# Kernel optimization log

Hardware: AMD Instinct MI355X
Metric: run time of the kernel (lower is better)

## Reference

```python
import jax, jax.numpy as jnp
import numpy as np

N = 100000
EPS_BN = 1e-5


def setup_inputs() -> dict:
    key = jax.random.key(0)
    ks = jax.random.split(key, 12)
    x = jax.random.normal(ks[0], (N, 128), dtype=jnp.float32)
    edge_index = jax.random.randint(ks[1], (2, 800000), 0, N, dtype=jnp.int64)
    # GCNConv layer params (PyG: lin weight [out,in], bias added after aggregation)
    s = 1.0 / np.sqrt(128.0)
    W1 = jax.random.uniform(ks[2], (128, 128), jnp.float32, -s, s)
    b1 = jnp.zeros((128,), jnp.float32)
    W2 = jax.random.uniform(ks[3], (128, 128), jnp.float32, -s, s)
    b2 = jnp.zeros((128,), jnp.float32)
    # BatchNorm affine params
    g1 = jnp.ones((128,), jnp.float32)
    be1 = jnp.zeros((128,), jnp.float32)
    g2 = jnp.ones((128,), jnp.float32)
    be2 = jnp.zeros((128,), jnp.float32)
    # PReLU single shared parameter (torch init = 0.25)
    a = jnp.asarray(0.25, jnp.float32)
    return {"x": x, "edge_index": edge_index, "W1": W1, "b1": b1, "g1": g1,
            "be1": be1, "W2": W2, "b2": b2, "g2": g2, "be2": be2, "a": a}


def _gcn_conv(x, src, dst, deg_inv_sqrt, W, b):
    # x' = D^-1/2 (A+I) D^-1/2 (x W^T) + b  (self loops already in src/dst)
    h = x @ W.T                                   # [N, out]
    norm = deg_inv_sqrt[src] * deg_inv_sqrt[dst]  # [E+N]
    msg = h[src] * norm[:, None]                  # gather + scale
    out = jax.ops.segment_sum(msg, dst, num_segments=N)  # scatter-add
    return out + b


def _batchnorm(x, g, be):
    # training-mode BatchNorm1d over nodes (biased variance)
    mean = jnp.mean(x, axis=0)
    var = jnp.mean(jnp.square(x - mean), axis=0)
    return (x - mean) * jax.lax.rsqrt(var + EPS_BN) * g + be


def _prelu(x, a):
    return jnp.where(x > 0, x, a * x)


def reference(x, edge_index, W1, b1, g1, be1, W2, b2, g2, be2, a):
    # add self loops
    loops = jnp.arange(N, dtype=edge_index.dtype)
    src = jnp.concatenate([edge_index[0], loops])
    dst = jnp.concatenate([edge_index[1], loops])
    # symmetric normalization from in-degree at destinations
    deg = jax.ops.segment_sum(jnp.ones_like(dst, dtype=x.dtype), dst, num_segments=N)
    deg_inv_sqrt = jnp.where(deg > 0, jax.lax.rsqrt(deg), 0.0)

    h = _gcn_conv(x, src, dst, deg_inv_sqrt, W1, b1)
    h = _prelu(_batchnorm(h, g1, be1), a)
    h = _gcn_conv(h, src, dst, deg_inv_sqrt, W2, b2)
    h = _prelu(_batchnorm(h, g2, be2), a)
    return h
```

## Files before the change

### kernel.cpp

```cpp
#include <hip/hip_runtime.h>
#include <cstddef>
#include <cstdint>


#define EPS_BN 1e-5f

typedef short short8 __attribute__((ext_vector_type(8)));
typedef float f32x4 __attribute__((ext_vector_type(4)));

static __device__ __forceinline__ unsigned short f2b(float f) {
    union { float f; uint32_t u; } v; v.f = f;
    uint32_t u = v.u;
    return (unsigned short)((u + 0x7FFFu + ((u >> 16) & 1u)) >> 16);
}
static __device__ __forceinline__ float b2f(unsigned short h) {
    union { uint32_t u; float f; } v; v.u = ((uint32_t)h) << 16;
    return v.f;
}
static __device__ __forceinline__ float b2f_s(short h) { return b2f((unsigned short)h); }

__global__ __launch_bounds__(256) void k_prep(const float* __restrict__ W1, const float* __restrict__ W2,
                                              unsigned short* __restrict__ Wz1, unsigned short* __restrict__ Wz2,
                                              const int* __restrict__ dst, int* __restrict__ cnt,
                                              int* __restrict__ rank, int E) {
    int bid = blockIdx.x, tid = threadIdx.x;
    if (bid < 128) {
        int gi = bid * 256 + tid;
        const float* W = (gi < 16384) ? W1 : W2;
        unsigned short* Wz = (gi < 16384) ? Wz1 : Wz2;
        int idx = gi & 16383;
        int o = idx >> 7, k = idx & 127;
        int ct = o >> 4, nn = o & 15, ks = k >> 5, q = (k >> 3) & 3, j = k & 7;
        Wz[(ct * 4 + ks) * 512 + (q * 16 + nn) * 8 + j] = f2b(W[idx]);
    } else {
        int e = (bid - 128) * 256 + tid;
        if (e < E) rank[e] = atomicAdd(&cnt[dst[e]], 1);
    }
}

__global__ __launch_bounds__(256) void k_scanA(const int* __restrict__ cnt, int* __restrict__ partial, int n) {
    __shared__ int sd[256];
    int tid = threadIdx.x;
    int base = blockIdx.x * 1024 + tid * 4;
    int s = 0;
#pragma unroll
    for (int j = 0; j < 4; j++) { int idx = base + j; if (idx < n) s += cnt[idx]; }
    sd[tid] = s; __syncthreads();
    for (int off = 128; off > 0; off >>= 1) {
        if (tid < off) sd[tid] += sd[tid + off];
        __syncthreads();
    }
    if (tid == 0) partial[blockIdx.x] = sd[0];
}

__global__ __launch_bounds__(256) void k_scanC(const int* __restrict__ cnt, const int* __restrict__ partial,
                                               int* __restrict__ rowptr, float* __restrict__ dis, int n, int nb) {
    __shared__ int sp[256];
    __shared__ int sd[256];
    int tid = threadIdx.x;
    sp[tid] = (tid < nb) ? partial[tid] : 0;
    int base = blockIdx.x * 1024 + tid * 4;
    int v[4]; int s = 0;
#pragma unroll
    for (int j = 0; j < 4; j++) { int idx = base + j; v[j] = (idx < n) ? cnt[idx] : 0; s += v[j]; }
    sd[tid] = s;
    __syncthreads();
    for (int off = 1; off < 256; off <<= 1) {
        int a = (tid >= off) ? sp[tid - off] : 0;
        int b = (tid >= off) ? sd[tid - off] : 0;
        __syncthreads();
        sp[tid] += a; sd[tid] += b;
        __syncthreads();
    }
    int gbase = (blockIdx.x == 0) ? 0 : sp[blockIdx.x - 1];
    int excl = gbase + ((tid == 0) ? 0 : sd[tid - 1]);
#pragma unroll
    for (int j = 0; j < 4; j++) {
        int idx = base + j;
        if (idx < n) {
            rowptr[idx] = excl;
            dis[idx] = rsqrtf((float)(v[j] + 1));
        }
        excl += v[j];
    }
}

__global__ __launch_bounds__(256) void k_fill_gemm1(const float* __restrict__ X,
                                                    const unsigned short* __restrict__ Wz,
                                                    unsigned short* __restrict__ Yb, int n,
                                                    const int* __restrict__ src, const int* __restrict__ dst,
                                                    const int* __restrict__ rowptr, const int* __restrict__ rank,
                                                    int* __restrict__ colw, int E, int gGemm) {
    __shared__ unsigned short lds[16384];
    int tid = threadIdx.x;
    if ((int)blockIdx.x >= gGemm) {
        int e = (blockIdx.x - gGemm) * 256 + tid;
        if (e < E) {
            int d = dst[e];
            colw[rowptr[d] + rank[e]] = src[e];
        }
        return;
    }
    const short8* wsrc = (const short8*)Wz;
    short8* ldst = (short8*)lds;
#pragma unroll
    for (int i = 0; i < 8; i++) ldst[tid + 256 * i] = wsrc[tid + 256 * i];
    __syncthreads();

    int wave = tid >> 6, lane = tid & 63;
    int r0 = blockIdx.x * 64 + wave * 16;
    int mrow = lane & 15, quad = lane >> 4;
    int arow = r0 + mrow; if (arow > n - 1) arow = n - 1;
    const float* xr = X + (size_t)arow * 128;

    f32x4 acc[8];
#pragma unroll
    for (int ct = 0; ct < 8; ct++) acc[ct] = (f32x4){0.f, 0.f, 0.f, 0.f};

#pragma unroll
    for (int ks = 0; ks < 4; ks++) {
        int kb = ks * 32 + quad * 8;
        float4 x0 = *reinterpret_cast<const float4*>(xr + kb);
        float4 x1 = *reinterpret_cast<const float4*>(xr + kb + 4);
        short8 a;
        a[0] = (short)f2b(x0.x); a[1] = (short)f2b(x0.y); a[2] = (short)f2b(x0.z); a[3] = (short)f2b(x0.w);
        a[4] = (short)f2b(x1.x); a[5] = (short)f2b(x1.y); a[6] = (short)f2b(x1.z); a[7] = (short)f2b(x1.w);
#pragma unroll
        for (int ct = 0; ct < 8; ct++) {
            short8 b = *(const short8*)(lds + (ct * 4 + ks) * 512 + lane * 8);
            acc[ct] = __builtin_amdgcn_mfma_f32_16x16x32_bf16(a, b, acc[ct], 0, 0, 0);
        }
    }
#pragma unroll
    for (int i = 0; i < 4; i++) {
        int row = r0 + quad * 4 + i;
        if (row < n) {
#pragma unroll
            for (int ct = 0; ct < 8; ct++)
                Yb[(size_t)row * 128 + ct * 16 + mrow] = f2b(acc[ct][i]);
        }
    }
}

__global__ __launch_bounds__(256) void k_gemm2(const unsigned short* __restrict__ Ab,
                                               const unsigned short* __restrict__ Wz,
                                               const float* __restrict__ acc1,
                                               const float* __restrict__ g1, const float* __restrict__ be1,
                                               const float* __restrict__ ap,
                                               unsigned short* __restrict__ Yb, float invN, int n) {
    __shared__ unsigned short lds[16384];
    __shared__ float scl[128];
    __shared__ float shl[128];
    int tid = threadIdx.x;
    if (tid < 128) {
        float mean = acc1[tid] * invN;
        float var = acc1[128 + tid] * invN - mean * mean;
        float rstd = rsqrtf(var + EPS_BN);
        float scale = g1[tid] * rstd;
        scl[tid] = scale;
        shl[tid] = fmaf(-mean, scale, be1[tid]);
    }
    const short8* wsrc = (const short8*)Wz;
    short8* ldst = (short8*)lds;
#pragma unroll
    for (int i = 0; i < 8; i++) ldst[tid + 256 * i] = wsrc[tid + 256 * i];
    __syncthreads();

    float alpha = ap[0];
    int wave = tid >> 6, lane = tid & 63;
    int r0 = blockIdx.x * 64 + wave * 16;
    int mrow = lane & 15, quad = lane >> 4;
    int arow = r0 + mrow; if (arow > n - 1) arow = n - 1;
    const unsigned short* ar = Ab + (size_t)arow * 128;

    f32x4 acc[8];
#pragma unroll
    for (int ct = 0; ct < 8; ct++) acc[ct] = (f32x4){0.f, 0.f, 0.f, 0.f};

#pragma unroll
    for (int ks = 0; ks < 4; ks++) {
        int kb = ks * 32 + quad * 8;
        short8 raw = *(const short8*)(ar + kb);
        float4 s0 = *reinterpret_cast<const float4*>(scl + kb);
        float4 s1 = *reinterpret_cast<const float4*>(scl + kb + 4);
        float4 t0 = *reinterpret_cast<const float4*>(shl + kb);
        float4 t1 = *reinterpret_cast<const float4*>(shl + kb + 4);
        float ss[8] = {s0.x, s0.y, s0.z, s0.w, s1.x, s1.y, s1.z, s1.w};
        float tt[8] = {t0.x, t0.y, t0.z, t0.w, t1.x, t1.y, t1.z, t1.w};
        short8 a;
#pragma unroll
        for (int j = 0; j < 8; j++) {
            float x = fmaf(b2f_s(raw[j]), ss[j], tt[j]);
            x = x > 0.f ? x : alpha * x;
            a[j] = (short)f2b(x);
        }
#pragma unroll
        for (int ct = 0; ct < 8; ct++) {
            short8 b = *(const short8*)(lds + (ct * 4 + ks) * 512 + lane * 8);
            acc[ct] = __builtin_amdgcn_mfma_f32_16x16x32_bf16(a, b, acc[ct], 0, 0, 0);
        }
    }
#pragma unroll
    for (int i = 0; i < 4; i++) {
        int row = r0 + quad * 4 + i;
        if (row < n) {
#pragma unroll
            for (int ct = 0; ct < 8; ct++)
                Yb[(size_t)row * 128 + ct * 16 + mrow] = f2b(acc[ct][i]);
        }
    }
}

__global__ __launch_bounds__(256) void k_aggst(const unsigned short* __restrict__ Hb,
                                               const int* __restrict__ rowptr, const int* __restrict__ cnt,
                                               const int* __restrict__ colw, const float* __restrict__ dis,
                                               const float* __restrict__ bias,
                                               unsigned short* __restrict__ outb,
                                               float* __restrict__ part, int n) {
    __shared__ float ls[4][128];
    __shared__ float lq[4][128];
    int tid = threadIdx.x;
    int lane = tid & 15, slot = tid >> 4;
    int node = blockIdx.x * 16 + slot;
    bool act = node < n;
    int nodec = act ? node : (n - 1);
    int lo = lane * 8;
    float dn = dis[nodec];
    short8 hv = *(const short8*)(Hb + (size_t)nodec * 128 + lo);
    float acc[8];
#pragma unroll
    for (int j = 0; j < 8; j++) acc[j] = dn * b2f_s(hv[j]);
    int num = act ? cnt[nodec] : 0;
    int beg = rowptr[nodec];
    const int* cw = colw + beg;
    int e = 0;
    for (; e + 4 <= num; e += 4) {
        int s0 = cw[e], s1 = cw[e + 1], s2 = cw[e + 2], s3 = cw[e + 3];
        float w0 = dis[s0], w1 = dis[s1], w2 = dis[s2], w3 = dis[s3];
        short8 n0 = *(const short8*)(Hb + (size_t)s0 * 128 + lo);
        short8 n1 = *(const short8*)(Hb + (size_t)s1 * 128 + lo);
        short8 n2 = *(const short8*)(Hb + (size_t)s2 * 128 + lo);
        short8 n3 = *(const short8*)(Hb + (size_t)s3 * 128 + lo);
#pragma unroll
        for (int j = 0; j < 8; j++) {
            acc[j] = fmaf(w0, b2f_s(n0[j]), acc[j]);
            acc[j] = fmaf(w1, b2f_s(n1[j]), acc[j]);
            acc[j] = fmaf(w2, b2f_s(n2[j]), acc[j]);
            acc[j] = fmaf(w3, b2f_s(n3[j]), acc[j]);
        }
    }
    for (; e < num; ++e) {
        int s = cw[e];
        float w = dis[s];
        short8 nb = *(const short8*)(Hb + (size_t)s * 128 + lo);
#pragma unroll
        for (int j = 0; j < 8; j++) acc[j] = fmaf(w, b2f_s(nb[j]), acc[j]);
    }
    const float4 bv0 = reinterpret_cast<const float4*>(bias)[lane * 2 + 0];
    const float4 bv1 = reinterpret_cast<const float4*>(bias)[lane * 2 + 1];
    float bb[8] = {bv0.x, bv0.y, bv0.z, bv0.w, bv1.x, bv1.y, bv1.z, bv1.w};
    short8 ov;
    float s8[8], q8[8];
#pragma unroll
    for (int j = 0; j < 8; j++) {
        float y = fmaf(dn, acc[j], bb[j]);
        unsigned short h = f2b(y);
        ov[j] = (short)h;
        float fv = act ? b2f(h) : 0.f;
        s8[j] = fv;
        q8[j] = fv * fv;
    }
    if (act) *(short8*)(outb + (size_t)node * 128 + lo) = ov;
#pragma unroll
    for (int j = 0; j < 8; j++) {
        s8[j] += __shfl_xor(s8[j], 16, 64);
        q8[j] += __shfl_xor(q8[j], 16, 64);
        s8[j] += __shfl_xor(s8[j], 32, 64);
        q8[j] += __shfl_xor(q8[j], 32, 64);
    }
    int wave = tid >> 6;
    if ((tid & 63) < 16) {
#pragma unroll
        for (int j = 0; j < 8; j++) {
            ls[wave][lane * 8 + j] = s8[j];
            lq[wave][lane * 8 + j] = q8[j];
        }
    }
    __syncthreads();
    if (tid < 128) {
        float r = ls[0][tid] + ls[1][tid] + ls[2][tid] + ls[3][tid];
        part[(size_t)blockIdx.x * 256 + tid] = r;
    } else {
        int f = tid - 128;
        float r = lq[0][f] + lq[1][f] + lq[2][f] + lq[3][f];
        part[(size_t)blockIdx.x * 256 + 128 + f] = r;
    }
}

__global__ __launch_bounds__(256) void k_bnred(const float* __restrict__ part, float* __restrict__ acc, int nb) {
    int tid = threadIdx.x;
    float s = 0.f;
    for (int b = blockIdx.x; b < nb; b += gridDim.x) s += part[(size_t)b * 256 + tid];
    atomicAdd(&acc[tid], s);
}

__global__ __launch_bounds__(256) void k_bnact_f(const unsigned short* __restrict__ X, float* __restrict__ Y,
                                                 const float* __restrict__ acc2,
                                                 const float* __restrict__ g2, const float* __restrict__ be2,
                                                 const float* __restrict__ ap, float invN, int n8) {
    __shared__ float scl[128];
    __shared__ float shl[128];
    int tid = threadIdx.x;
    if (tid < 128) {
        float mean = acc2[tid] * invN;
        float var = acc2[128 + tid] * invN - mean * mean;
        float rstd = rsqrtf(var + EPS_BN);
        float scale = g2[tid] * rstd;
        scl[tid] = scale;
        shl[tid] = fmaf(-mean, scale, be2[tid]);
    }
    __syncthreads();
    int i = blockIdx.x * 256 + tid;
    if (i >= n8) return;
    float a = ap[0];
    int g = i & 15;
    const float4 s0 = reinterpret_cast<const float4*>(scl)[g * 2 + 0];
    const float4 s1 = reinterpret_cast<const float4*>(scl)[g * 2 + 1];
    const float4 t0 = reinterpret_cast<const float4*>(shl)[g * 2 + 0];
    const float4 t1 = reinterpret_cast<const float4*>(shl)[g * 2 + 1];
    float ss[8] = {s0.x, s0.y, s0.z, s0.w, s1.x, s1.y, s1.z, s1.w};
    float tt[8] = {t0.x, t0.y, t0.z, t0.w, t1.x, t1.y, t1.z, t1.w};
    short8 v = reinterpret_cast<const short8*>(X)[i];
    float out[8];
#pragma unroll
    for (int j = 0; j < 8; j++) {
        float x = fmaf(b2f_s(v[j]), ss[j], tt[j]);
        out[j] = x > 0.f ? x : a * x;
    }
    float4 o0 = {out[0], out[1], out[2], out[3]};
    float4 o1 = {out[4], out[5], out[6], out[7]};
    reinterpret_cast<float4*>(Y)[i * 2 + 0] = o0;
    reinterpret_cast<float4*>(Y)[i * 2 + 1] = o1;
}

extern "C" void kernel_launch(void* const* d_in, const int* in_sizes, int n_in,
                              void* d_out, int out_size, void* d_ws, size_t ws_size,
                              hipStream_t stream) {
    (void)n_in; (void)out_size; (void)ws_size;
    const float* x   = (const float*)d_in[0];
    const int*   ei  = (const int*)d_in[1];
    const float* W1  = (const float*)d_in[2];
    const float* b1  = (const float*)d_in[3];
    const float* g1  = (const float*)d_in[4];
    const float* be1 = (const float*)d_in[5];
    const float* W2  = (const float*)d_in[6];
    const float* b2  = (const float*)d_in[7];
    const float* g2  = (const float*)d_in[8];
    const float* be2 = (const float*)d_in[9];
    const float* ap  = (const float*)d_in[10];
    float* out = (float*)d_out;

    const int N = in_sizes[0] / 128;
    const int E = in_sizes[1] / 2;
    const int* srcIdx = ei;
    const int* dstIdx = ei + E;

    const int NB = (N + 1023) / 1024;
    const int gE = (E + 255) / 256;
    const int n8 = N * 16;
    const int gGemm = (N + 63) / 64;
    const int gAgg  = (N + 15) / 16;

    char* w = (char*)d_ws;
    size_t off = 0;
    auto alloc = [&](size_t bytes) { char* p = w + off; off += (bytes + 255) & ~(size_t)255; return p; };
    int*   cnt     = (int*)  alloc((size_t)N * 4);
    float* acc1    = (float*)alloc(1024);
    float* acc2    = (float*)alloc(1024);
    size_t zero_bytes = off;
    int*   rowptr  = (int*)  alloc((size_t)N * 4);
    int*   rank    = (int*)  alloc((size_t)E * 4);
    int*   colw    = (int*)  alloc((size_t)E * 4);
    float* dis     = (float*)alloc((size_t)N * 4);
    int*   partial = (int*)  alloc(4096);
    float* part    = (float*)alloc((size_t)gAgg * 256 * 4);
    unsigned short* Wz1 = (unsigned short*)alloc(16384 * 2);
    unsigned short* Wz2 = (unsigned short*)alloc(16384 * 2);
    unsigned short* bufH = (unsigned short*)alloc((size_t)N * 128 * 2);
    unsigned short* bufA = (unsigned short*)alloc((size_t)N * 128 * 2);

    const float invN = 1.0f / (float)N;

    hipMemsetAsync(cnt, 0, zero_bytes, stream);

    k_prep<<<128 + gE, 256, 0, stream>>>(W1, W2, Wz1, Wz2, dstIdx, cnt, rank, E);

    k_scanA<<<NB, 256, 0, stream>>>(cnt, partial, N);
    k_scanC<<<NB, 256, 0, stream>>>(cnt, partial, rowptr, dis, N, NB);

    k_fill_gemm1<<<gGemm + gE, 256, 0, stream>>>(x, Wz1, bufH, N,
                                                 srcIdx, dstIdx, rowptr, rank, colw, E, gGemm);
    k_aggst<<<gAgg, 256, 0, stream>>>(bufH, rowptr, cnt, colw, dis, b1, bufA, part, N);
    k_bnred<<<64, 256, 0, stream>>>(part, acc1, gAgg);

    k_gemm2<<<gGemm, 256, 0, stream>>>(bufA, Wz2, acc1, g1, be1, ap, bufH, invN, N);
    k_aggst<<<gAgg, 256, 0, stream>>>(bufH, rowptr, cnt, colw, dis, b2, bufA, part, N);
    k_bnred<<<64, 256, 0, stream>>>(part, acc2, gAgg);
    k_bnact_f<<<(n8 + 255) / 256, 256, 0, stream>>>(bufA, out, acc2, g2, be2, ap, invN, n8);
}
```

Before: 342.2 us.

## Fuse all stages into one persistent cooperative kernel with grid syncs

Replaces the chain of separate kernel launches (prep, scans, fill+GEMM1, aggregation, BN reduction, GEMM2, final BN/act) with a single cooperative persistent kernel that uses grid-wide barriers between phases and grid-stride loops. BN statistics are now accumulated per block across many nodes and atomically added directly, removing the partials buffer and the separate reduction kernels. This is meant to remove launch gaps and the extra partials traffic, but it adds grid.sync costs, limits the grid to occupancy-bound block counts, and uses a large static LDS allocation that may reduce occupancy. The scan phases now run on only a few blocks while all others wait at the barrier.

```diff
diff --git a/kernel.cpp b/kernel.cpp
--- a/kernel.cpp
+++ b/kernel.cpp
@@ -1,9 +1,12 @@
 #include <hip/hip_runtime.h>
+#include <hip/hip_cooperative_groups.h>
 #include <cstddef>
 #include <cstdint>
 
 
 #define EPS_BN 1e-5f
+
+namespace cg = cooperative_groups;
 
 typedef short short8 __attribute__((ext_vector_type(8)));
 typedef float f32x4 __attribute__((ext_vector_type(4)));
@@ -19,328 +22,336 @@
 }
 static __device__ __forceinline__ float b2f_s(short h) { return b2f((unsigned short)h); }
 
-__global__ __launch_bounds__(256) void k_prep(const float* __restrict__ W1, const float* __restrict__ W2,
-                                              unsigned short* __restrict__ Wz1, unsigned short* __restrict__ Wz2,
-                                              const int* __restrict__ dst, int* __restrict__ cnt,
-                                              int* __restrict__ rank, int E) {
-    int bid = blockIdx.x, tid = threadIdx.x;
-    if (bid < 128) {
-        int gi = bid * 256 + tid;
-        const float* W = (gi < 16384) ? W1 : W2;
-        unsigned short* Wz = (gi < 16384) ? Wz1 : Wz2;
+struct Args {
+    const float* x;
+    const int* src;
+    const int* dst;
+    const float* W1; const float* b1; const float* g1; const float* be1;
+    const float* W2; const float* b2; const float* g2; const float* be2;
+    const float* ap;
+    float* out;
+    int* cnt; float* acc1; float* acc2;
+    int* rowptr; int* rank; int* colw; float* dis; int* partial;
+    unsigned short* Wz1; unsigned short* Wz2;
+    unsigned short* bufH; unsigned short* bufA;
+    int N, E, NB, nTiles, gAgg, n8;
+    float invN;
+};
+
+static __device__ __forceinline__ void agg_phase(const Args& a,
+                                                 const unsigned short* __restrict__ Hb,
+                                                 const float* __restrict__ bias,
+                                                 unsigned short* __restrict__ outb,
+                                                 float* __restrict__ accg,
+                                                 unsigned char* smem,
+                                                 int tid, int bid, int nBlocks) {
+    float rs[8], rq[8];
+#pragma unroll
+    for (int j = 0; j < 8; j++) { rs[j] = 0.f; rq[j] = 0.f; }
+    int lane = tid & 15, slot = tid >> 4;
+    int lo = lane * 8;
+    const float4 bv0 = reinterpret_cast<const float4*>(bias)[lane * 2 + 0];
+    const float4 bv1 = reinterpret_cast<const float4*>(bias)[lane * 2 + 1];
+    float bb[8] = {bv0.x, bv0.y, bv0.z, bv0.w, bv1.x, bv1.y, bv1.z, bv1.w};
+
+    for (int gb = bid; gb < a.gAgg; gb += nBlocks) {
+        int node = gb * 16 + slot;
+        bool act = node < a.N;
+        int nodec = act ? node : (a.N - 1);
+        float dn = a.dis[nodec];
+        short8 hv = *(const short8*)(Hb + (size_t)nodec * 128 + lo);
+        float acc[8];
+#pragma unroll
+        for (int j = 0; j < 8; j++) acc[j] = dn * b2f_s(hv[j]);
+        int num = act ? a.cnt[nodec] : 0;
+        int beg = a.rowptr[nodec];
+        const int* cw = a.colw + beg;
+        int e = 0;
+        for (; e + 4 <= num; e += 4) {
+            int s0 = cw[e], s1 = cw[e + 1], s2 = cw[e + 2], s3 = cw[e + 3];
+            float w0 = a.dis[s0], w1 = a.dis[s1], w2 = a.dis[s2], w3 = a.dis[s3];
+            short8 n0 = *(const short8*)(Hb + (size_t)s0 * 128 + lo);
+            short8 n1 = *(const short8*)(Hb + (size_t)s1 * 128 + lo);
+            short8 n2 = *(const short8*)(Hb + (size_t)s2 * 128 + lo);
+            short8 n3 = *(const short8*)(Hb + (size_t)s3 * 128 + lo);
+#pragma unroll
+            for (int j = 0; j < 8; j++) {
+                acc[j] = fmaf(w0, b2f_s(n0[j]), acc[j]);
+                acc[j] = fmaf(w1, b2f_s(n1[j]), acc[j]);
+                acc[j] = fmaf(w2, b2f_s(n2[j]), acc[j]);
+                acc[j] = fmaf(w3, b2f_s(n3[j]), acc[j]);
+            }
+        }
+        for (; e < num; ++e) {
+            int s = cw[e];
+            float w = a.dis[s];
+            short8 nb = *(const short8*)(Hb + (size_t)s * 128 + lo);
+#pragma unroll
+            for (int j = 0; j < 8; j++) acc[j] = fmaf(w, b2f_s(nb[j]), acc[j]);
+        }
+        short8 ov;
+#pragma unroll
+        for (int j = 0; j < 8; j++) {
+            float y = fmaf(dn, acc[j], bb[j]);
+            unsigned short h = f2b(y);
+            ov[j] = (short)h;
+            float fv = act ? b2f(h) : 0.f;
+            rs[j] += fv;
+            rq[j] = fmaf(fv, fv, rq[j]);
+        }
+        if (act) *(short8*)(outb + (size_t)node * 128 + lo) = ov;
+    }
+#pragma unroll
+    for (int j = 0; j < 8; j++) {
+        rs[j] += __shfl_xor(rs[j], 16, 64);
+        rq[j] += __shfl_xor(rq[j], 16, 64);
+        rs[j] += __shfl_xor(rs[j], 32, 64);
+        rq[j] += __shfl_xor(rq[j], 32, 64);
+    }
+    float* lsf = (float*)smem;
+    float* lqf = lsf + 512;
+    int wv = tid >> 6;
+    __syncthreads();
+    if ((tid & 63) < 16) {
+#pragma unroll
+        for (int j = 0; j < 8; j++) {
+            lsf[wv * 128 + lane * 8 + j] = rs[j];
+            lqf[wv * 128 + lane * 8 + j] = rq[j];
+        }
+    }
+    __syncthreads();
+    if (tid < 128) {
+        atomicAdd(&accg[tid], lsf[tid] + lsf[128 + tid] + lsf[256 + tid] + lsf[384 + tid]);
+    } else {
+        int f = tid - 128;
+        atomicAdd(&accg[tid], lqf[f] + lqf[128 + f] + lqf[256 + f] + lqf[384 + f]);
+    }
+}
+
+__global__ __launch_bounds__(256, 4) void k_mega(Args a) {
+    cg::grid_group grid = cg::this_grid();
+    __shared__ __align__(16) unsigned char smem[33792];
+    int tid = threadIdx.x;
+    int bid = blockIdx.x;
+    int nBlocks = gridDim.x;
+    int gtid = bid * 256 + tid;
+    int gth = nBlocks * 256;
+
+    for (int gi = gtid; gi < 32768; gi += gth) {
+        const float* W = (gi < 16384) ? a.W1 : a.W2;
+        unsigned short* Wz = (gi < 16384) ? a.Wz1 : a.Wz2;
         int idx = gi & 16383;
         int o = idx >> 7, k = idx & 127;
         int ct = o >> 4, nn = o & 15, ks = k >> 5, q = (k >> 3) & 3, j = k & 7;
         Wz[(ct * 4 + ks) * 512 + (q * 16 + nn) * 8 + j] = f2b(W[idx]);
-    } else {
-        int e = (bid - 128) * 256 + tid;
-        if (e < E) rank[e] = atomicAdd(&cnt[dst[e]], 1);
-    }
-}
-
-__global__ __launch_bounds__(256) void k_scanA(const int* __restrict__ cnt, int* __restrict__ partial, int n) {
-    __shared__ int sd[256];
-    int tid = threadIdx.x;
-    int base = blockIdx.x * 1024 + tid * 4;
-    int s = 0;
-#pragma unroll
-    for (int j = 0; j < 4; j++) { int idx = base + j; if (idx < n) s += cnt[idx]; }
-    sd[tid] = s; __syncthreads();
-    for (int off = 128; off > 0; off >>= 1) {
-        if (tid < off) sd[tid] += sd[tid + off];
+    }
+    for (int e = gtid; e < a.E; e += gth)
+        a.rank[e] = atomicAdd(&a.cnt[a.dst[e]], 1);
+    grid.sync();
+
+    {
+        int* sdI = (int*)smem;
+        for (int v = bid; v < a.NB; v += nBlocks) {
+            int base = v * 1024 + tid * 4;
+            int s = 0;
+#pragma unroll
+            for (int j = 0; j < 4; j++) { int idx = base + j; if (idx < a.N) s += a.cnt[idx]; }
+            sdI[tid] = s; __syncthreads();
+            for (int off = 128; off > 0; off >>= 1) {
+                if (tid < off) sdI[tid] += sdI[tid + off];
+                __syncthreads();
+            }
+            if (tid == 0) a.partial[v] = sdI[0];
+            __syncthreads();
+        }
+    }
+    grid.sync();
+
+    {
+        int* sp = (int*)smem;
+        int* sd = sp + 256;
+        for (int v = bid; v < a.NB; v += nBlocks) {
+            sp[tid] = (tid < a.NB) ? a.partial[tid] : 0;
+            int base = v * 1024 + tid * 4;
+            int vv[4]; int s = 0;
+#pragma unroll
+            for (int j = 0; j < 4; j++) { int idx = base + j; vv[j] = (idx < a.N) ? a.cnt[idx] : 0; s += vv[j]; }
+            sd[tid] = s;
+            __syncthreads();
+            for (int off = 1; off < 256; off <<= 1) {
+                int A = (tid >= off) ? sp[tid - off] : 0;
+                int B = (tid >= off) ? sd[tid - off] : 0;
+                __syncthreads();
+                sp[tid] += A; sd[tid] += B;
+                __syncthreads();
+            }
+            int gbase = (v == 0) ? 0 : sp[v - 1];
+            int excl = gbase + ((tid == 0) ? 0 : sd[tid - 1]);
+#pragma unroll
+            for (int j = 0; j < 4; j++) {
+                int idx = base + j;
+                if (idx < a.N) {
+                    a.rowptr[idx] = excl;
+                    a.dis[idx] = rsqrtf((float)(vv[j] + 1));
+                }
+                excl += vv[j];
+            }
+            __syncthreads();
+        }
+    }
+    grid.sync();
+
+    for (int e = gtid; e < a.E; e += gth) {
+        int d = a.dst[e];
+        a.colw[a.rowptr[d] + a.rank[e]] = a.src[e];
+    }
+    {
+        short8* lds8 = (short8*)smem;
+        const short8* wsrc = (const short8*)a.Wz1;
+#pragma unroll
+        for (int i = 0; i < 8; i++) lds8[tid + 256 * i] = wsrc[tid + 256 * i];
         __syncthreads();
-    }
-    if (tid == 0) partial[blockIdx.x] = sd[0];
-}
-
-__global__ __launch_bounds__(256) void k_scanC(const int* __restrict__ cnt, const int* __restrict__ partial,
-                                               int* __restrict__ rowptr, float* __restrict__ dis, int n, int nb) {
-    __shared__ int sp[256];
-    __shared__ int sd[256];
-    int tid = threadIdx.x;
-    sp[tid] = (tid < nb) ? partial[tid] : 0;
-    int base = blockIdx.x * 1024 + tid * 4;
-    int v[4]; int s = 0;
-#pragma unroll
-    for (int j = 0; j < 4; j++) { int idx = base + j; v[j] = (idx < n) ? cnt[idx] : 0; s += v[j]; }
-    sd[tid] = s;
-    __syncthreads();
-    for (int off = 1; off < 256; off <<= 1) {
-        int a = (tid >= off) ? sp[tid - off] : 0;
-        int b = (tid >= off) ? sd[tid - off] : 0;
+        unsigned short* ldsu = (unsigned short*)smem;
+        int wave = tid >> 6, lane = tid & 63;
+        int mrow = lane & 15, quad = lane >> 4;
+        for (int t = bid; t < a.nTiles; t += nBlocks) {
+            int r0 = t * 64 + wave * 16;
+            int arow = r0 + mrow; if (arow > a.N - 1) arow = a.N - 1;
+            const float* xr = a.x + (size_t)arow * 128;
+            f32x4 acc[8];
+#pragma unroll
+            for (int ct = 0; ct < 8; ct++) acc[ct] = (f32x4){0.f, 0.f, 0.f, 0.f};
+#pragma unroll
+            for (int ks = 0; ks < 4; ks++) {
+                int kb = ks * 32 + quad * 8;
+                float4 x0 = *reinterpret_cast<const float4*>(xr + kb);
+                float4 x1 = *reinterpret_cast<const float4*>(xr + kb + 4);
+                short8 av;
+                av[0] = (short)f2b(x0.x); av[1] = (short)f2b(x0.y); av[2] = (short)f2b(x0.z); av[3] = (short)f2b(x0.w);
+                av[4] = (short)f2b(x1.x); av[5] = (short)f2b(x1.y); av[6] = (short)f2b(x1.z); av[7] = (short)f2b(x1.w);
+#pragma unroll
+                for (int ct = 0; ct < 8; ct++) {
+                    short8 b = *(const short8*)(ldsu + (ct * 4 + ks) * 512 + lane * 8);
+                    acc[ct] = __builtin_amdgcn_mfma_f32_16x16x32_bf16(av, b, acc[ct], 0, 0, 0);
+                }
+            }
+#pragma unroll
+            for (int i = 0; i < 4; i++) {
+                int row = r0 + quad * 4 + i;
+                if (row < a.N) {
+#pragma unroll
+                    for (int ct = 0; ct < 8; ct++)
+                        a.bufH[(size_t)row * 128 + ct * 16 + mrow] = f2b(acc[ct][i]);
+                }
+            }
+        }
+    }
+    grid.sync();
+
+    agg_phase(a, a.bufH, a.b1, a.bufA, a.acc1, smem, tid, bid, nBlocks);
+    grid.sync();
+
+    {
+        float* scl = (float*)(smem + 32768);
+        float* shl = scl + 128;
+        if (tid < 128) {
+            float mean = a.acc1[tid] * a.invN;
+            float var = a.acc1[128 + tid] * a.invN - mean * mean;
+            float rstd = rsqrtf(var + EPS_BN);
+            float sc = a.g1[tid] * rstd;
+            scl[tid] = sc;
+            shl[tid] = fmaf(-mean, sc, a.be1[tid]);
+        }
+        short8* lds8 = (short8*)smem;
+        const short8* wsrc = (const short8*)a.Wz2;
+#pragma unroll
+        for (int i = 0; i < 8; i++) lds8[tid + 256 * i] = wsrc[tid + 256 * i];
         __syncthreads();
-        sp[tid] += a; sd[tid] += b;
+        unsigned short* ldsu = (unsigned short*)smem;
+        float alpha = a.ap[0];
+        int wave = tid >> 6, lane = tid & 63;
+        int mrow = lane & 15, quad = lane >> 4;
+        for (int t = bid; t < a.nTiles; t += nBlocks) {
+            int r0 = t * 64 + wave * 16;
+            int arow = r0 + mrow; if (arow > a.N - 1) arow = a.N - 1;
+            const unsigned short* ar = a.bufA + (size_t)arow * 128;
+            f32x4 acc[8];
+#pragma unroll
+            for (int ct = 0; ct < 8; ct++) acc[ct] = (f32x4){0.f, 0.f, 0.f, 0.f};
+#pragma unroll
+            for (int ks = 0; ks < 4; ks++) {
+                int kb = ks * 32 + quad * 8;
+                short8 raw = *(const short8*)(ar + kb);
+                float4 s0 = *reinterpret_cast<const float4*>(scl + kb);
+                float4 s1 = *reinterpret_cast<const float4*>(scl + kb + 4);
+                float4 t0 = *reinterpret_cast<const float4*>(shl + kb);
+                float4 t1 = *reinterpret_cast<const float4*>(shl + kb + 4);
+                float ss[8] = {s0.x, s0.y, s0.z, s0.w, s1.x, s1.y, s1.z, s1.w};
+                float tt[8] = {t0.x, t0.y, t0.z, t0.w, t1.x, t1.y, t1.z, t1.w};
+                short8 av;
+#pragma unroll
+                for (int j = 0; j < 8; j++) {
+                    float xv = fmaf(b2f_s(raw[j]), ss[j], tt[j]);
+                    xv = xv > 0.f ? xv : alpha * xv;
+                    av[j] = (short)f2b(xv);
+                }
+#pragma unroll
+                for (int ct = 0; ct < 8; ct++) {
+                    short8 b = *(const short8*)(ldsu + (ct * 4 + ks) * 512 + lane * 8);
+                    acc[ct] = __builtin_amdgcn_mfma_f32_16x16x32_bf16(av, b, acc[ct], 0, 0, 0);
+                }
+            }
+#pragma unroll
+            for (int i = 0; i < 4; i++) {
+                int row = r0 + quad * 4 + i;
+                if (row < a.N) {
+#pragma unroll
+                    for (int ct = 0; ct < 8; ct++)
+                        a.bufH[(size_t)row * 128 + ct * 16 + mrow] = f2b(acc[ct][i]);
+                }
+            }
+        }
+    }
+    grid.sync();
+
+    agg_phase(a, a.bufH, a.b2, a.bufA, a.acc2, smem, tid, bid, nBlocks);
+    grid.sync();
+
+    {
+        float* scl = (float*)smem;
+        float* shl = scl + 128;
         __syncthreads();
-    }
-    int gbase = (blockIdx.x == 0) ? 0 : sp[blockIdx.x - 1];
-    int excl = gbase + ((tid == 0) ? 0 : sd[tid - 1]);
-#pragma unroll
-    for (int j = 0; j < 4; j++) {
-        int idx = base + j;
-        if (idx < n) {
-            rowptr[idx] = excl;
-            dis[idx] = rsqrtf((float)(v[j] + 1));
-        }
-        excl += v[j];
-    }
-}
-
-__global__ __launch_bounds__(256) void k_fill_gemm1(const float* __restrict__ X,
-                                                    const unsigned short* __restrict__ Wz,
-                                                    unsigned short* __restrict__ Yb, int n,
-                                                    const int* __restrict__ src, const int* __restrict__ dst,
-                                                    const int* __restrict__ rowptr, const int* __restrict__ rank,
-                                                    int* __restrict__ colw, int E, int gGemm) {
-    __shared__ unsigned short lds[16384];
-    int tid = threadIdx.x;
-    if ((int)blockIdx.x >= gGemm) {
-        int e = (blockIdx.x - gGemm) * 256 + tid;
-        if (e < E) {
-            int d = dst[e];
-            colw[rowptr[d] + rank[e]] = src[e];
-        }
-        return;
-    }
-    const short8* wsrc = (const short8*)Wz;
-    short8* ldst = (short8*)lds;
-#pragma unroll
-    for (int i = 0; i < 8; i++) ldst[tid + 256 * i] = wsrc[tid + 256 * i];
-    __syncthreads();
-
-    int wave = tid >> 6, lane = tid & 63;
-    int r0 = blockIdx.x * 64 + wave * 16;
-    int mrow = lane & 15, quad = lane >> 4;
-    int arow = r0 + mrow; if (arow > n - 1) arow = n - 1;
-    const float* xr = X + (size_t)arow * 128;
-
-    f32x4 acc[8];
-#pragma unroll
-    for (int ct = 0; ct < 8; ct++) acc[ct] = (f32x4){0.f, 0.f, 0.f, 0.f};
-
-#pragma unroll
-    for (int ks = 0; ks < 4; ks++) {
-        int kb = ks * 32 + quad * 8;
-        float4 x0 = *reinterpret_cast<const float4*>(xr + kb);
-        float4 x1 = *reinterpret_cast<const float4*>(xr + kb + 4);
-        short8 a;
-        a[0] = (short)f2b(x0.x); a[1] = (short)f2b(x0.y); a[2] = (short)f2b(x0.z); a[3] = (short)f2b(x0.w);
-        a[4] = (short)f2b(x1.x); a[5] = (short)f2b(x1.y); a[6] = (short)f2b(x1.z); a[7] = (short)f2b(x1.w);
-#pragma unroll
-        for (int ct = 0; ct < 8; ct++) {
-            short8 b = *(const short8*)(lds + (ct * 4 + ks) * 512 + lane * 8);
-            acc[ct] = __builtin_amdgcn_mfma_f32_16x16x32_bf16(a, b, acc[ct], 0, 0, 0);
-        }
-    }
-#pragma unroll
-    for (int i = 0; i < 4; i++) {
-        int row = r0 + quad * 4 + i;
-        if (row < n) {
-#pragma unroll
-            for (int ct = 0; ct < 8; ct++)
-                Yb[(size_t)row * 128 + ct * 16 + mrow] = f2b(acc[ct][i]);
-        }
-    }
-}
-
-__global__ __launch_bounds__(256) void k_gemm2(const unsigned short* __restrict__ Ab,
-                                               const unsigned short* __restrict__ Wz,
-                                               const float* __restrict__ acc1,
-                                               const float* __restrict__ g1, const float* __restrict__ be1,
-                                               const float* __restrict__ ap,
-                                               unsigned short* __restrict__ Yb, float invN, int n) {
-    __shared__ unsigned short lds[16384];
-    __shared__ float scl[128];
-    __shared__ float shl[128];
-    int tid = threadIdx.x;
-    if (tid < 128) {
-        float mean = acc1[tid] * invN;
-        float var = acc1[128 + tid] * invN - mean * mean;
-        float rstd = rsqrtf(var + EPS_BN);
-        float scale = g1[tid] * rstd;
-        scl[tid] = scale;
-        shl[tid] = fmaf(-mean, scale, be1[tid]);
-    }
-    const short8* wsrc = (const short8*)Wz;
-    short8* ldst = (short8*)lds;
-#pragma unroll
-    for (int i = 0; i < 8; i++) ldst[tid + 256 * i] = wsrc[tid + 256 * i];
-    __syncthreads();
-
-    float alpha = ap[0];
-    int wave = tid >> 6, lane = tid & 63;
-    int r0 = blockIdx.x * 64 + wave * 16;
-    int mrow = lane & 15, quad = lane >> 4;
-    int arow = r0 + mrow; if (arow > n - 1) arow = n - 1;
-    const unsigned short* ar = Ab + (size_t)arow * 128;
-
-    f32x4 acc[8];
-#pragma unroll
-    for (int ct = 0; ct < 8; ct++) acc[ct] = (f32x4){0.f, 0.f, 0.f, 0.f};
-
-#pragma unroll
-    for (int ks = 0; ks < 4; ks++) {
-        int kb = ks * 32 + quad * 8;
-        short8 raw = *(const short8*)(ar + kb);
-        float4 s0 = *reinterpret_cast<const float4*>(scl + kb);
-        float4 s1 = *reinterpret_cast<const float4*>(scl + kb + 4);
-        float4 t0 = *reinterpret_cast<const float4*>(shl + kb);
-        float4 t1 = *reinterpret_cast<const float4*>(shl + kb + 4);
-        float ss[8] = {s0.x, s0.y, s0.z, s0.w, s1.x, s1.y, s1.z, s1.w};
-        float tt[8] = {t0.x, t0.y, t0.z, t0.w, t1.x, t1.y, t1.z, t1.w};
-        short8 a;
-#pragma unroll
-        for (int j = 0; j < 8; j++) {
-            float x = fmaf(b2f_s(raw[j]), ss[j], tt[j]);
-            x = x > 0.f ? x : alpha * x;
-            a[j] = (short)f2b(x);
-        }
-#pragma unroll
-        for (int ct = 0; ct < 8; ct++) {
-            short8 b = *(const short8*)(lds + (ct * 4 + ks) * 512 + lane * 8);
-            acc[ct] = __builtin_amdgcn_mfma_f32_16x16x32_bf16(a, b, acc[ct], 0, 0, 0);
-        }
-    }
-#pragma unroll
-    for (int i = 0; i < 4; i++) {
-        int row = r0 + quad * 4 + i;
-        if (row < n) {
-#pragma unroll
-            for (int ct = 0; ct < 8; ct++)
-                Yb[(size_t)row * 128 + ct * 16 + mrow] = f2b(acc[ct][i]);
-        }
-    }
-}
-
-__global__ __launch_bounds__(256) void k_aggst(const unsigned short* __restrict__ Hb,
-                                               const int* __restrict__ rowptr, const int* __restrict__ cnt,
-                                               const int* __restrict__ colw, const float* __restrict__ dis,
-                                               const float* __restrict__ bias,
-                                               unsigned short* __restrict__ outb,
-                                               float* __restrict__ part, int n) {
-    __shared__ float ls[4][128];
-    __shared__ float lq[4][128];
-    int tid = threadIdx.x;
-    int lane = tid & 15, slot = tid >> 4;
-    int node = blockIdx.x * 16 + slot;
-    bool act = node < n;
-    int nodec = act ? node : (n - 1);
-    int lo = lane * 8;
-    float dn = dis[nodec];
-    short8 hv = *(const short8*)(Hb + (size_t)nodec * 128 + lo);
-    float acc[8];
-#pragma unroll
-    for (int j = 0; j < 8; j++) acc[j] = dn * b2f_s(hv[j]);
-    int num = act ? cnt[nodec] : 0;
-    int beg = rowptr[nodec];
-    const int* cw = colw + beg;
-    int e = 0;
-    for (; e + 4 <= num; e += 4) {
-        int s0 = cw[e], s1 = cw[e + 1], s2 = cw[e + 2], s3 = cw[e + 3];
-        float w0 = dis[s0], w1 = dis[s1], w2 = dis[s2], w3 = dis[s3];
-        short8 n0 = *(const short8*)(Hb + (size_t)s0 * 128 + lo);
-        short8 n1 = *(const short8*)(Hb + (size_t)s1 * 128 + lo);
-        short8 n2 = *(const short8*)(Hb + (size_t)s2 * 128 + lo);
-        short8 n3 = *(const short8*)(Hb + (size_t)s3 * 128 + lo);
-#pragma unroll
-        for (int j = 0; j < 8; j++) {
-            acc[j] = fmaf(w0, b2f_s(n0[j]), acc[j]);
-            acc[j] = fmaf(w1, b2f_s(n1[j]), acc[j]);
-            acc[j] = fmaf(w2, b2f_s(n2[j]), acc[j]);
-            acc[j] = fmaf(w3, b2f_s(n3[j]), acc[j]);
-        }
-    }
-    for (; e < num; ++e) {
-        int s = cw[e];
-        float w = dis[s];
-        short8 nb = *(const short8*)(Hb + (size_t)s * 128 + lo);
-#pragma unroll
-        for (int j = 0; j < 8; j++) acc[j] = fmaf(w, b2f_s(nb[j]), acc[j]);
-    }
-    const float4 bv0 = reinterpret_cast<const float4*>(bias)[lane * 2 + 0];
-    const float4 bv1 = reinterpret_cast<const float4*>(bias)[lane * 2 + 1];
-    float bb[8] = {bv0.x, bv0.y, bv0.z, bv0.w, bv1.x, bv1.y, bv1.z, bv1.w};
-    short8 ov;
-    float s8[8], q8[8];
-#pragma unroll
-    for (int j = 0; j < 8; j++) {
-        float y = fmaf(dn, acc[j], bb[j]);
-        unsigned short h = f2b(y);
-        ov[j] = (short)h;
-        float fv = act ? b2f(h) : 0.f;
-        s8[j] = fv;
-        q8[j] = fv * fv;
-    }
-    if (act) *(short8*)(outb + (size_t)node * 128 + lo) = ov;
-#pragma unroll
-    for (int j = 0; j < 8; j++) {
-        s8[j] += __shfl_xor(s8[j], 16, 64);
-        q8[j] += __shfl_xor(q8[j], 16, 64);
-        s8[j] += __shfl_xor(s8[j], 32, 64);
-        q8[j] += __shfl_xor(q8[j], 32, 64);
-    }
-    int wave = tid >> 6;
-    if ((tid & 63) < 16) {
-#pragma unroll
-        for (int j = 0; j < 8; j++) {
-            ls[wave][lane * 8 + j] = s8[j];
-            lq[wave][lane * 8 + j] = q8[j];
-        }
-    }
-    __syncthreads();
-    if (tid < 128) {
-        float r = ls[0][tid] + ls[1][tid] + ls[2][tid] + ls[3][tid];
-        part[(size_t)blockIdx.x * 256 + tid] = r;
-    } else {
-        int f = tid - 128;
-        float r = lq[0][f] + lq[1][f] + lq[2][f] + lq[3][f];
-        part[(size_t)blockIdx.x * 256 + 128 + f] = r;
-    }
-}
-
-__global__ __launch_bounds__(256) void k_bnred(const float* __restrict__ part, float* __restrict__ acc, int nb) {
-    int tid = threadIdx.x;
-    float s = 0.f;
-    for (int b = blockIdx.x; b < nb; b += gridDim.x) s += part[(size_t)b * 256 + tid];
-    atomicAdd(&acc[tid], s);
-}
-
-__global__ __launch_bounds__(256) void k_bnact_f(const unsigned short* __restrict__ X, float* __restrict__ Y,
-                                                 const float* __restrict__ acc2,
-                                                 const float* __restrict__ g2, const float* __restrict__ be2,
-                                                 const float* __restrict__ ap, float invN, int n8) {
-    __shared__ float scl[128];
-    __shared__ float shl[128];
-    int tid = threadIdx.x;
-    if (tid < 128) {
-        float mean = acc2[tid] * invN;
-        float var = acc2[128 + tid] * invN - mean * mean;
-        float rstd = rsqrtf(var + EPS_BN);
-        float scale = g2[tid] * rstd;
-        scl[tid] = scale;
-        shl[tid] = fmaf(-mean, scale, be2[tid]);
-    }
-    __syncthreads();
-    int i = blockIdx.x * 256 + tid;
-    if (i >= n8) return;
-    float a = ap[0];
-    int g = i & 15;
-    const float4 s0 = reinterpret_cast<const float4*>(scl)[g * 2 + 0];
-    const float4 s1 = reinterpret_cast<const float4*>(scl)[g * 2 + 1];
-    const float4 t0 = reinterpret_cast<const float4*>(shl)[g * 2 + 0];
-    const float4 t1 = reinterpret_cast<const float4*>(shl)[g * 2 + 1];
-    float ss[8] = {s0.x, s0.y, s0.z, s0.w, s1.x, s1.y, s1.z, s1.w};
-    float tt[8] = {t0.x, t0.y, t0.z, t0.w, t1.x, t1.y, t1.z, t1.w};
-    short8 v = reinterpret_cast<const short8*>(X)[i];
-    float out[8];
-#pragma unroll
-    for (int j = 0; j < 8; j++) {
-        float x = fmaf(b2f_s(v[j]), ss[j], tt[j]);
-        out[j] = x > 0.f ? x : a * x;
-    }
-    float4 o0 = {out[0], out[1], out[2], out[3]};
-    float4 o1 = {out[4], out[5], out[6], out[7]};
-    reinterpret_cast<float4*>(Y)[i * 2 + 0] = o0;
-    reinterpret_cast<float4*>(Y)[i * 2 + 1] = o1;
+        if (tid < 128) {
+            float mean = a.acc2[tid] * a.invN;
+            float var = a.acc2[128 + tid] * a.invN - mean * mean;
+            float rstd = rsqrtf(var + EPS_BN);
+            float sc = a.g2[tid] * rstd;
+            scl[tid] = sc;
+            shl[tid] = fmaf(-mean, sc, a.be2[tid]);
+        }
+        __syncthreads();
+        float alpha = a.ap[0];
+        for (int i = gtid; i < a.n8; i += gth) {
+            int g = i & 15;
+            const float4 s0 = reinterpret_cast<const float4*>(scl)[g * 2 + 0];
+            const float4 s1 = reinterpret_cast<const float4*>(scl)[g * 2 + 1];
+            const float4 t0 = reinterpret_cast<const float4*>(shl)[g * 2 + 0];
+            const float4 t1 = reinterpret_cast<const float4*>(shl)[g * 2 + 1];
+            float ss[8] = {s0.x, s0.y, s0.z, s0.w, s1.x, s1.y, s1.z, s1.w};
+            float tt[8] = {t0.x, t0.y, t0.z, t0.w, t1.x, t1.y, t1.z, t1.w};
+            short8 v = reinterpret_cast<const short8*>(a.bufA)[i];
+            float outv[8];
+#pragma unroll
+            for (int j = 0; j < 8; j++) {
+                float xv = fmaf(b2f_s(v[j]), ss[j], tt[j]);
+                outv[j] = xv > 0.f ? xv : alpha * xv;
+            }
+            float4 o0 = {outv[0], outv[1], outv[2], outv[3]};
+            float4 o1 = {outv[4], outv[5], outv[6], outv[7]};
+            reinterpret_cast<float4*>(a.out)[i * 2 + 0] = o0;
+            reinterpret_cast<float4*>(a.out)[i * 2 + 1] = o1;
+        }
+    }
 }
 
 extern "C" void kernel_launch(void* const* d_in, const int* in_sizes, int n_in,
@@ -349,27 +360,14 @@
     (void)n_in; (void)out_size; (void)ws_size;
     const float* x   = (const float*)d_in[0];
     const int*   ei  = (const int*)d_in[1];
-    const float* W1  = (const float*)d_in[2];
-    const float* b1  = (const float*)d_in[3];
-    const float* g1  = (const float*)d_in[4];
-    const float* be1 = (const float*)d_in[5];
-    const float* W2  = (const float*)d_in[6];
-    const float* b2  = (const float*)d_in[7];
-    const float* g2  = (const float*)d_in[8];
-    const float* be2 = (const float*)d_in[9];
-    const float* ap  = (const float*)d_in[10];
-    float* out = (float*)d_out;
 
     const int N = in_sizes[0] / 128;
     const int E = in_sizes[1] / 2;
-    const int* srcIdx = ei;
-    const int* dstIdx = ei + E;
 
     const int NB = (N + 1023) / 1024;
-    const int gE = (E + 255) / 256;
+    const int nTiles = (N + 63) / 64;
+    const int gAgg = (N + 15) / 16;
     const int n8 = N * 16;
-    const int gGemm = (N + 63) / 64;
-    const int gAgg  = (N + 15) / 16;
 
     char* w = (char*)d_ws;
     size_t off = 0;
@@ -383,28 +381,35 @@
     int*   colw    = (int*)  alloc((size_t)E * 4);
     float* dis     = (float*)alloc((size_t)N * 4);
     int*   partial = (int*)  alloc(4096);
-    float* part    = (float*)alloc((size_t)gAgg * 256 * 4);
     unsigned short* Wz1 = (unsigned short*)alloc(16384 * 2);
     unsigned short* Wz2 = (unsigned short*)alloc(16384 * 2);
     unsigned short* bufH = (unsigned short*)alloc((size_t)N * 128 * 2);
     unsigned short* bufA = (unsigned short*)alloc((size_t)N * 128 * 2);
 
-    const float invN = 1.0f / (float)N;
+    Args a;
+    a.x = x;
+    a.src = ei;
+    a.dst = ei + E;
+    a.W1 = (const float*)d_in[2];  a.b1 = (const float*)d_in[3];
+    a.g1 = (const float*)d_in[4];  a.be1 = (const float*)d_in[5];
+    a.W2 = (const float*)d_in[6];  a.b2 = (const float*)d_in[7];
+    a.g2 = (const float*)d_in[8];  a.be2 = (const float*)d_in[9];
+    a.ap = (const float*)d_in[10];
+    a.out = (float*)d_out;
+    a.cnt = cnt; a.acc1 = acc1; a.acc2 = acc2;
+    a.rowptr = rowptr; a.rank = rank; a.colw = colw; a.dis = dis; a.partial = partial;
+    a.Wz1 = Wz1; a.Wz2 = Wz2; a.bufH = bufH; a.bufA = bufA;
+    a.N = N; a.E = E; a.NB = NB; a.nTiles = nTiles; a.gAgg = gAgg; a.n8 = n8;
+    a.invN = 1.0f / (float)N;
 
     hipMemsetAsync(cnt, 0, zero_bytes, stream);
 
-    k_prep<<<128 + gE, 256, 0, stream>>>(W1, W2, Wz1, Wz2, dstIdx, cnt, rank, E);
-
-    k_scanA<<<NB, 256, 0, stream>>>(cnt, partial, N);
-    k_scanC<<<NB, 256, 0, stream>>>(cnt, partial, rowptr, dis, N, NB);
-
-    k_fill_gemm1<<<gGemm + gE, 256, 0, stream>>>(x, Wz1, bufH, N,
-                                                 srcIdx, dstIdx, rowptr, rank, colw, E, gGemm);
-    k_aggst<<<gAgg, 256, 0, stream>>>(bufH, rowptr, cnt, colw, dis, b1, bufA, part, N);
-    k_bnred<<<64, 256, 0, stream>>>(part, acc1, gAgg);
-
-    k_gemm2<<<gGemm, 256, 0, stream>>>(bufA, Wz2, acc1, g1, be1, ap, bufH, invN, N);
-    k_aggst<<<gAgg, 256, 0, stream>>>(bufH, rowptr, cnt, colw, dis, b2, bufA, part, N);
-    k_bnred<<<64, 256, 0, stream>>>(part, acc2, gAgg);
-    k_bnact_f<<<(n8 + 255) / 256, 256, 0, stream>>>(bufA, out, acc2, g2, be2, ap, invN, n8);
+    int occ = 0;
+    hipOccupancyMaxActiveBlocksPerMultiprocessor(&occ, k_mega, 256, 0);
+    if (occ < 1) occ = 1;
+    int nBlocks = occ * 256;
+    if (nBlocks > 2048) nBlocks = 2048;
+
+    void* kargs[] = { (void*)&a };
+    hipLaunchCooperativeKernel(k_mega, dim3(nBlocks), dim3(256), kargs, 0, stream);
 }
```

Result: slower. 828.5 us (+142.1%).
